# Optimization experiments

Measured on AMD Instinct MI355X. Metric: run time of the kernel, lower is better.

## Reference

```python
import jax, jax.numpy as jnp
import numpy as np

N = 100000
E = 1250000
D = 64
POS_DIM = 3


def _linear_params(key, fan_in, fan_out, bias=True):
    k1, k2 = jax.random.split(key)
    bound = 1.0 / np.sqrt(fan_in)
    W = jax.random.uniform(k1, (fan_in, fan_out), minval=-bound, maxval=bound, dtype=jnp.float32)
    if bias:
        b = jax.random.uniform(k2, (fan_out,), minval=-bound, maxval=bound, dtype=jnp.float32)
        return W, b
    return W


def setup_inputs() -> dict:
    key = jax.random.key(0)
    ks = jax.random.split(key, 10)
    x = jax.random.normal(ks[0], (N, D), dtype=jnp.float32)
    pos = jax.random.normal(ks[1], (N, POS_DIM), dtype=jnp.float32)
    edge_index = jax.random.randint(ks[2], (2, E), 0, N, dtype=jnp.int64)
    W_in, b_in = _linear_params(ks[3], D, D)
    W_lin = _linear_params(ks[4], D, D, bias=False)
    W_src = _linear_params(ks[5], D, D, bias=False)
    W_dst = _linear_params(ks[6], D, D, bias=False)
    W_pos, b_pos = _linear_params(ks[7], POS_DIM, D)
    W_out, b_out = _linear_params(ks[8], D, D)
    return {"x": x, "pos": pos, "edge_index": edge_index,
            "W_in": W_in, "b_in": b_in, "W_lin": W_lin, "W_src": W_src,
            "W_dst": W_dst, "W_pos": W_pos, "b_pos": b_pos,
            "W_out": W_out, "b_out": b_out}


def reference(x, pos, edge_index, W_in, b_in, W_lin, W_src, W_dst, W_pos, b_pos, W_out, b_out):
    n = x.shape[0]
    src, dst = edge_index[0], edge_index[1]  # j, i (PyG source_to_target)
    # lin_in + relu
    h = jax.nn.relu(x @ W_in + b_in)  # [N, D]
    # PointTransformerConv projections
    x_lin = h @ W_lin      # value projection, gathered at src (x_j)
    a_src = h @ W_src      # alpha_j side
    a_dst = h @ W_dst      # alpha_i side
    # per-edge positional MLP on pos_i - pos_j
    delta = (pos[dst] - pos[src]) @ W_pos + b_pos  # [E, D]
    # per-edge attention logits, per channel
    alpha = a_dst[dst] - a_src[src] + delta  # [E, D]
    # segment softmax over destination node groups (PyG softmax, eps=1e-16)
    seg_max = jax.ops.segment_max(alpha, dst, num_segments=n)
    alpha = jnp.exp(alpha - seg_max[dst])
    seg_sum = jax.ops.segment_sum(alpha, dst, num_segments=n)
    alpha = alpha / (seg_sum[dst] + 1e-16)
    # weighted messages, scatter-add aggregate
    msg = alpha * (x_lin[src] + delta)  # [E, D]
    out = jax.ops.segment_sum(msg, dst, num_segments=n)  # [N, D]
    # lin_out + relu
    return jax.nn.relu(out @ W_out + b_out)
```

## Files before the change

### kernel.cpp

```cpp
#include <hip/hip_runtime.h>

#define NN 100000
#define NE 1250000
#define NWIN 782
#define GA 256
#define CHUNK ((NE + GA - 1) / GA)
#define CAP 32
#define WEDCAP 40

typedef __attribute__((ext_vector_type(4))) float f32x4;
typedef __attribute__((ext_vector_type(8))) short s16x8;

__device__ __forceinline__ short bfb(float f) {
    union { float f; unsigned u; } c; c.f = f;
    unsigned u = c.u + 0x7fffu + ((c.u >> 16) & 1u);
    return (short)(u >> 16);
}
__device__ __forceinline__ void splitbf(float v, short& hi, short& lo) {
    hi = bfb(v);
    union { unsigned u; float f; } c; c.u = ((unsigned)(unsigned short)hi) << 16;
    lo = bfb(v - c.f);
}
__device__ __forceinline__ float lo2f(unsigned u) {
    union { unsigned u; float f; } c; c.u = u << 16; return c.f;
}
__device__ __forceinline__ float hi2f(unsigned u) {
    union { unsigned u; float f; } c; c.u = u & 0xffff0000u; return c.f;
}

__global__ __launch_bounds__(256) void k_prep(
    const float* __restrict__ Wi, const float* __restrict__ Wl,
    const float* __restrict__ Ws, const float* __restrict__ Wo,
    short* __restrict__ P)
{
    const int t = blockIdx.x * 256 + threadIdx.x;
    if (t >= 2048) return;
    const int mat = t >> 9, rem = t & 511;
    const int lane = rem & 63, cfg = rem >> 6;
    const int kh = cfg >> 2, nt = cfg & 3;
    const int m = lane & 15, q = lane >> 4;
    const float* W = mat == 0 ? Wi : mat == 1 ? Wl : mat == 2 ? Ws : Wo;
    s16x8 v;
    #pragma unroll
    for (int i = 0; i < 8; ++i)
        v[i] = bfb(W[(kh * 32 + q * 8 + i) * 64 + nt * 16 + m]);
    *(s16x8*)&P[(size_t)t * 8] = v;
}

__global__ __launch_bounds__(256) void k_node_in(
    const float* __restrict__ x, const short* __restrict__ P,
    const float* __restrict__ b_in, unsigned* __restrict__ AXb)
{
    __shared__ float hT[4][16 * 68];
    const int lane = threadIdx.x & 63;
    const int wid  = threadIdx.x >> 6;
    const int m = lane & 15, q = lane >> 4;

    s16x8 Wf[3][2][4];
    #pragma unroll
    for (int mat = 0; mat < 3; ++mat)
        #pragma unroll
        for (int kh = 0; kh < 2; ++kh)
            #pragma unroll
            for (int nt = 0; nt < 4; ++nt)
                Wf[mat][kh][nt] = *(const s16x8*)&P[((size_t)mat * 512 + (kh * 4 + nt) * 64 + lane) * 8];
    float bin[4];
    #pragma unroll
    for (int nt = 0; nt < 4; ++nt) bin[nt] = b_in[nt * 16 + m];

    const int wave = blockIdx.x * 4 + wid, nw = gridDim.x * 4;
    for (int chunk = wave; chunk < NN / 16; chunk += nw) {
        const int r0 = chunk * 16;
        const float* xr = x + (size_t)(r0 + m) * 64;
        float xv[16];
        *(float4*)&xv[0]  = *(const float4*)(xr + q * 8);
        *(float4*)&xv[4]  = *(const float4*)(xr + q * 8 + 4);
        *(float4*)&xv[8]  = *(const float4*)(xr + 32 + q * 8);
        *(float4*)&xv[12] = *(const float4*)(xr + 32 + q * 8 + 4);
        s16x8 ahi0, alo0, ahi1, alo1;
        #pragma unroll
        for (int i = 0; i < 8; ++i) {
            short h, l;
            splitbf(xv[i], h, l);     ahi0[i] = h; alo0[i] = l;
            splitbf(xv[8 + i], h, l); ahi1[i] = h; alo1[i] = l;
        }
        #pragma unroll
        for (int nt = 0; nt < 4; ++nt) {
            f32x4 acc = {0.f, 0.f, 0.f, 0.f};
            acc = __builtin_amdgcn_mfma_f32_16x16x32_bf16(alo0, Wf[0][0][nt], acc, 0, 0, 0);
            acc = __builtin_amdgcn_mfma_f32_16x16x32_bf16(alo1, Wf[0][1][nt], acc, 0, 0, 0);
            acc = __builtin_amdgcn_mfma_f32_16x16x32_bf16(ahi0, Wf[0][0][nt], acc, 0, 0, 0);
            acc = __builtin_amdgcn_mfma_f32_16x16x32_bf16(ahi1, Wf[0][1][nt], acc, 0, 0, 0);
            #pragma unroll
            for (int r = 0; r < 4; ++r) {
                float hv = acc[r] + bin[nt];
                hT[wid][(q * 4 + r) * 68 + nt * 16 + m] = hv > 0.f ? hv : 0.f;
            }
        }
        float hv[16];
        *(float4*)&hv[0]  = *(const float4*)&hT[wid][m * 68 + q * 8];
        *(float4*)&hv[4]  = *(const float4*)&hT[wid][m * 68 + q * 8 + 4];
        *(float4*)&hv[8]  = *(const float4*)&hT[wid][m * 68 + 32 + q * 8];
        *(float4*)&hv[12] = *(const float4*)&hT[wid][m * 68 + 32 + q * 8 + 4];
        s16x8 hhi0, hlo0, hhi1, hlo1;
        #pragma unroll
        for (int i = 0; i < 8; ++i) {
            short h, l;
            splitbf(hv[i], h, l);     hhi0[i] = h; hlo0[i] = l;
            splitbf(hv[8 + i], h, l); hhi1[i] = h; hlo1[i] = l;
        }
        #pragma unroll
        for (int nt = 0; nt < 4; ++nt) {
            f32x4 aS = {0.f, 0.f, 0.f, 0.f}, aL = {0.f, 0.f, 0.f, 0.f};
            aS = __builtin_amdgcn_mfma_f32_16x16x32_bf16(hlo0, Wf[2][0][nt], aS, 0, 0, 0);
            aS = __builtin_amdgcn_mfma_f32_16x16x32_bf16(hlo1, Wf[2][1][nt], aS, 0, 0, 0);
            aS = __builtin_amdgcn_mfma_f32_16x16x32_bf16(hhi0, Wf[2][0][nt], aS, 0, 0, 0);
            aS = __builtin_amdgcn_mfma_f32_16x16x32_bf16(hhi1, Wf[2][1][nt], aS, 0, 0, 0);
            aL = __builtin_amdgcn_mfma_f32_16x16x32_bf16(hlo0, Wf[1][0][nt], aL, 0, 0, 0);
            aL = __builtin_amdgcn_mfma_f32_16x16x32_bf16(hlo1, Wf[1][1][nt], aL, 0, 0, 0);
            aL = __builtin_amdgcn_mfma_f32_16x16x32_bf16(hhi0, Wf[1][0][nt], aL, 0, 0, 0);
            aL = __builtin_amdgcn_mfma_f32_16x16x32_bf16(hhi1, Wf[1][1][nt], aL, 0, 0, 0);
            #pragma unroll
            for (int r = 0; r < 4; ++r) {
                const unsigned p = (unsigned)(unsigned short)bfb(aS[r])
                                 | ((unsigned)(unsigned short)bfb(aL[r]) << 16);
                AXb[(size_t)(r0 + q * 4 + r) * 64 + nt * 16 + m] = p;
            }
        }
    }
}

__global__ __launch_bounds__(256) void k_passA(
    const int* __restrict__ ei, unsigned* __restrict__ stage, int* __restrict__ gcnt)
{
    __shared__ int lcnt[NWIN];
    const int g = blockIdx.x;
    for (int i = threadIdx.x; i < NWIN; i += 256) lcnt[i] = 0;
    __syncthreads();
    const int e0 = g * CHUNK;
    const int e1 = (e0 + CHUNK < NE) ? e0 + CHUNK : NE;
    for (int e = e0 + threadIdx.x; e < e1; e += 256) {
        const int s = ei[e], d = ei[NE + e];
        const int b = d >> 7;
        const int c = atomicAdd(&lcnt[b], 1);
        if (c < CAP)
            stage[((size_t)b * GA + g) * CAP + c] = (unsigned)s | ((unsigned)(d & 127) << 17);
    }
    __syncthreads();
    for (int i = threadIdx.x; i < NWIN; i += 256) gcnt[i * GA + g] = lcnt[i];
}

__global__ __launch_bounds__(256) void k_passB(
    const unsigned* __restrict__ stage, const int* __restrict__ gcnt,
    int* __restrict__ slots, int* __restrict__ deg)
{
    __shared__ int slotsL[128 * WEDCAP];
    __shared__ int cntL[128];
    const int b = blockIdx.x;
    const int t = threadIdx.x;
    if (t < 128) cntL[t] = 0;
    __syncthreads();
    int n = gcnt[b * GA + t]; n = n < CAP ? n : CAP;
    const unsigned* cell = stage + ((size_t)b * GA + t) * CAP;
    for (int i = 0; i < n; ++i) {
        const unsigned ent = cell[i];
        const int d7 = (int)(ent >> 17);
        const int c = atomicAdd(&cntL[d7], 1);
        if (c < WEDCAP) slotsL[d7 * WEDCAP + c] = (int)(ent & 0x1ffff);
    }
    __syncthreads();
    int4* dstq = (int4*)(slots + (size_t)b * 128 * WEDCAP);
    const int4* srcq = (const int4*)slotsL;
    #pragma unroll
    for (int i = 0; i < 5; ++i) dstq[i * 256 + t] = srcq[i * 256 + t];
    if (t < 128) {
        const int d = (b << 7) + t;
        if (d < NN) deg[d] = cntL[t] < WEDCAP ? cntL[t] : WEDCAP;
    }
}

__global__ __launch_bounds__(256) void k_agg(
    const int* __restrict__ deg_arr, const int* __restrict__ slots,
    const float* __restrict__ pos,
    const float* __restrict__ W_pos, const float* __restrict__ b_pos,
    const unsigned* __restrict__ AXb, float* __restrict__ V)
{
    const int lane = threadIdx.x & 63;
    const int d = __builtin_amdgcn_readfirstlane((int)((blockIdx.x * 256 + threadIdx.x) >> 6));
    if (d >= NN) return;
    const float wp0 = W_pos[lane], wp1 = W_pos[64 + lane], wp2 = W_pos[128 + lane];
    const float bp  = b_pos[lane];
    const float pd0 = pos[d * 3 + 0], pd1 = pos[d * 3 + 1], pd2 = pos[d * 3 + 2];

    int deg = deg_arr[d]; deg = deg < WEDCAP ? deg : WEDCAP;
    const int* srow = slots + (size_t)d * WEDCAP;

    float Sa = 0.f, Ua = 0.f;
    if (deg > 0) {
        int cs[4], ns[4];
        float cpx[4], cpy[4], cpz[4], npx[4], npy[4], npz[4];
        unsigned cax[4], nax[4];
        {
            const int4 qd = *(const int4*)srow;
            cs[0] = qd.x;
            cs[1] = (1 < deg) ? qd.y : qd.x;
            cs[2] = (2 < deg) ? qd.z : qd.x;
            cs[3] = (3 < deg) ? qd.w : qd.x;
            #pragma unroll
            for (int k = 0; k < 4; ++k) {
                cpx[k] = pos[cs[k] * 3 + 0];
                cpy[k] = pos[cs[k] * 3 + 1];
                cpz[k] = pos[cs[k] * 3 + 2];
                cax[k] = AXb[(size_t)cs[k] * 64 + lane];
            }
        }
        for (int j = 0; j < deg; j += 8) {
            if (j + 4 < deg) {
                const int4 qd = *(const int4*)(srow + j + 4);
                ns[0] = qd.x;
                ns[1] = (j + 5 < deg) ? qd.y : qd.x;
                ns[2] = (j + 6 < deg) ? qd.z : qd.x;
                ns[3] = (j + 7 < deg) ? qd.w : qd.x;
                #pragma unroll
                for (int k = 0; k < 4; ++k) {
                    npx[k] = pos[ns[k] * 3 + 0];
                    npy[k] = pos[ns[k] * 3 + 1];
                    npz[k] = pos[ns[k] * 3 + 2];
                    nax[k] = AXb[(size_t)ns[k] * 64 + lane];
                }
            }
            #pragma unroll
            for (int k = 0; k < 4; ++k) {
                const float dl = fmaf(pd0 - cpx[k], wp0,
                                 fmaf(pd1 - cpy[k], wp1,
                                 fmaf(pd2 - cpz[k], wp2, bp)));
                float wv = __expf(dl - lo2f(cax[k]));
                if (j + k >= deg) wv = 0.f;
                Sa += wv;
                Ua = fmaf(wv, hi2f(cax[k]) + dl, Ua);
            }
            if (j + 8 < deg) {
                const int4 qd = *(const int4*)(srow + j + 8);
                cs[0] = qd.x;
                cs[1] = (j + 9  < deg) ? qd.y : qd.x;
                cs[2] = (j + 10 < deg) ? qd.z : qd.x;
                cs[3] = (j + 11 < deg) ? qd.w : qd.x;
                #pragma unroll
                for (int k = 0; k < 4; ++k) {
                    cpx[k] = pos[cs[k] * 3 + 0];
                    cpy[k] = pos[cs[k] * 3 + 1];
                    cpz[k] = pos[cs[k] * 3 + 2];
                    cax[k] = AXb[(size_t)cs[k] * 64 + lane];
                }
            }
            if (j + 4 < deg) {
                #pragma unroll
                for (int k = 0; k < 4; ++k) {
                    const float dl = fmaf(pd0 - npx[k], wp0,
                                     fmaf(pd1 - npy[k], wp1,
                                     fmaf(pd2 - npz[k], wp2, bp)));
                    float wv = __expf(dl - lo2f(nax[k]));
                    if (j + 4 + k >= deg) wv = 0.f;
                    Sa += wv;
                    Ua = fmaf(wv, hi2f(nax[k]) + dl, Ua);
                }
            }
        }
    }
    V[(size_t)d * 64 + lane] = Ua / (Sa + 1e-16f);
}

__global__ __launch_bounds__(256) void k_node_out(
    const float* __restrict__ V, const short* __restrict__ P,
    const float* __restrict__ b_out, float* __restrict__ out)
{
    const int lane = threadIdx.x & 63;
    const int wid  = threadIdx.x >> 6;
    const int m = lane & 15, q = lane >> 4;

    s16x8 Wf[2][4];
    #pragma unroll
    for (int kh = 0; kh < 2; ++kh)
        #pragma unroll
        for (int nt = 0; nt < 4; ++nt)
            Wf[kh][nt] = *(const s16x8*)&P[((size_t)3 * 512 + (kh * 4 + nt) * 64 + lane) * 8];
    float bo[4];
    #pragma unroll
    for (int nt = 0; nt < 4; ++nt) bo[nt] = b_out[nt * 16 + m];

    const int wave = blockIdx.x * 4 + wid, nw = gridDim.x * 4;
    for (int chunk = wave; chunk < NN / 16; chunk += nw) {
        const int r0 = chunk * 16;
        const float* vr = V + (size_t)(r0 + m) * 64;
        float vv[16];
        *(float4*)&vv[0]  = *(const float4*)(vr + q * 8);
        *(float4*)&vv[4]  = *(const float4*)(vr + q * 8 + 4);
        *(float4*)&vv[8]  = *(const float4*)(vr + 32 + q * 8);
        *(float4*)&vv[12] = *(const float4*)(vr + 32 + q * 8 + 4);
        s16x8 ahi0, alo0, ahi1, alo1;
        #pragma unroll
        for (int i = 0; i < 8; ++i) {
            short h, l;
            splitbf(vv[i], h, l);     ahi0[i] = h; alo0[i] = l;
            splitbf(vv[8 + i], h, l); ahi1[i] = h; alo1[i] = l;
        }
        #pragma unroll
        for (int nt = 0; nt < 4; ++nt) {
            f32x4 acc = {0.f, 0.f, 0.f, 0.f};
            acc = __builtin_amdgcn_mfma_f32_16x16x32_bf16(alo0, Wf[0][nt], acc, 0, 0, 0);
            acc = __builtin_amdgcn_mfma_f32_16x16x32_bf16(alo1, Wf[1][nt], acc, 0, 0, 0);
            acc = __builtin_amdgcn_mfma_f32_16x16x32_bf16(ahi0, Wf[0][nt], acc, 0, 0, 0);
            acc = __builtin_amdgcn_mfma_f32_16x16x32_bf16(ahi1, Wf[1][nt], acc, 0, 0, 0);
            #pragma unroll
            for (int r = 0; r < 4; ++r) {
                float o = acc[r] + bo[nt];
                out[(size_t)(r0 + q * 4 + r) * 64 + nt * 16 + m] = o > 0.f ? o : 0.f;
            }
        }
    }
}

extern "C" void kernel_launch(void* const* d_in, const int* in_sizes, int n_in,
                              void* d_out, int out_size, void* d_ws, size_t ws_size,
                              hipStream_t stream) {
    const float* x     = (const float*)d_in[0];
    const float* pos   = (const float*)d_in[1];
    const int*   ei    = (const int*)d_in[2];
    const float* W_in  = (const float*)d_in[3];
    const float* b_in  = (const float*)d_in[4];
    const float* W_lin = (const float*)d_in[5];
    const float* W_src = (const float*)d_in[6];
    const float* W_pos = (const float*)d_in[8];
    const float* b_pos = (const float*)d_in[9];
    const float* W_out = (const float*)d_in[10];
    const float* b_out = (const float*)d_in[11];

    unsigned* AXb   = (unsigned*)d_ws;
    unsigned* stage = AXb + (size_t)NN * 64;
    int*      gcnt  = (int*)(stage + (size_t)NWIN * GA * CAP);
    int*      slots = gcnt + (size_t)NWIN * GA;
    int*      deg   = slots + (size_t)NWIN * 128 * WEDCAP;
    float*    V     = (float*)(deg + NN);
    short*    P     = (short*)(V + (size_t)NN * 64);

    k_prep    <<<8,    256, 0, stream>>>(W_in, W_lin, W_src, W_out, P);
    k_node_in <<<512,  256, 0, stream>>>(x, P, b_in, AXb);
    k_passA   <<<GA,   256, 0, stream>>>(ei, stage, gcnt);
    k_passB   <<<NWIN, 256, 0, stream>>>(stage, gcnt, slots, deg);
    k_agg     <<<(NN + 3) / 4, 256, 0, stream>>>(deg, slots, pos, W_pos, b_pos, AXb, V);
    k_node_out<<<512,  256, 0, stream>>>(V, P, b_out, (float*)d_out);
}
```

Before: 216.0 us.

## Fuse edge aggregation with output projection into one kernel per 16-node tile

Merges the per-node aggregation and the output linear+ReLU kernels. Each wave now aggregates 16 consecutive nodes sequentially, transposes them through shared memory, and applies the MFMA output projection directly. This removes the intermediate V buffer write/read and one launch. In exchange the grid shrinks 16x and each wave runs 16 serial latency-bound gather loops, reducing memory-level parallelism.

```diff
diff --git a/kernel.cpp b/kernel.cpp
--- a/kernel.cpp
+++ b/kernel.cpp
@@ -179,72 +179,54 @@
     }
 }
 
-__global__ __launch_bounds__(256) void k_agg(
+__global__ __launch_bounds__(256) void k_aggout(
     const int* __restrict__ deg_arr, const int* __restrict__ slots,
     const float* __restrict__ pos,
     const float* __restrict__ W_pos, const float* __restrict__ b_pos,
-    const unsigned* __restrict__ AXb, float* __restrict__ V)
-{
+    const unsigned* __restrict__ AXb,
+    const short* __restrict__ P, const float* __restrict__ b_out,
+    float* __restrict__ out)
+{
+    __shared__ float hT[4][16 * 68];
     const int lane = threadIdx.x & 63;
-    const int d = __builtin_amdgcn_readfirstlane((int)((blockIdx.x * 256 + threadIdx.x) >> 6));
-    if (d >= NN) return;
+    const int wid  = threadIdx.x >> 6;
+    const int m = lane & 15, q = lane >> 4;
+
+    const int gid = blockIdx.x * 4 + wid;
+    if (gid >= NN / 16) return;
+    const int dbase = gid * 16;
+
     const float wp0 = W_pos[lane], wp1 = W_pos[64 + lane], wp2 = W_pos[128 + lane];
     const float bp  = b_pos[lane];
-    const float pd0 = pos[d * 3 + 0], pd1 = pos[d * 3 + 1], pd2 = pos[d * 3 + 2];
-
-    int deg = deg_arr[d]; deg = deg < WEDCAP ? deg : WEDCAP;
-    const int* srow = slots + (size_t)d * WEDCAP;
-
-    float Sa = 0.f, Ua = 0.f;
-    if (deg > 0) {
-        int cs[4], ns[4];
-        float cpx[4], cpy[4], cpz[4], npx[4], npy[4], npz[4];
-        unsigned cax[4], nax[4];
-        {
-            const int4 qd = *(const int4*)srow;
-            cs[0] = qd.x;
-            cs[1] = (1 < deg) ? qd.y : qd.x;
-            cs[2] = (2 < deg) ? qd.z : qd.x;
-            cs[3] = (3 < deg) ? qd.w : qd.x;
-            #pragma unroll
-            for (int k = 0; k < 4; ++k) {
-                cpx[k] = pos[cs[k] * 3 + 0];
-                cpy[k] = pos[cs[k] * 3 + 1];
-                cpz[k] = pos[cs[k] * 3 + 2];
-                cax[k] = AXb[(size_t)cs[k] * 64 + lane];
-            }
-        }
-        for (int j = 0; j < deg; j += 8) {
-            if (j + 4 < deg) {
-                const int4 qd = *(const int4*)(srow + j + 4);
-                ns[0] = qd.x;
-                ns[1] = (j + 5 < deg) ? qd.y : qd.x;
-                ns[2] = (j + 6 < deg) ? qd.z : qd.x;
-                ns[3] = (j + 7 < deg) ? qd.w : qd.x;
-                #pragma unroll
-                for (int k = 0; k < 4; ++k) {
-                    npx[k] = pos[ns[k] * 3 + 0];
-                    npy[k] = pos[ns[k] * 3 + 1];
-                    npz[k] = pos[ns[k] * 3 + 2];
-                    nax[k] = AXb[(size_t)ns[k] * 64 + lane];
-                }
-            }
-            #pragma unroll
-            for (int k = 0; k < 4; ++k) {
-                const float dl = fmaf(pd0 - cpx[k], wp0,
-                                 fmaf(pd1 - cpy[k], wp1,
-                                 fmaf(pd2 - cpz[k], wp2, bp)));
-                float wv = __expf(dl - lo2f(cax[k]));
-                if (j + k >= deg) wv = 0.f;
-                Sa += wv;
-                Ua = fmaf(wv, hi2f(cax[k]) + dl, Ua);
-            }
-            if (j + 8 < deg) {
-                const int4 qd = *(const int4*)(srow + j + 8);
+    s16x8 Wf[2][4];
+    #pragma unroll
+    for (int kh = 0; kh < 2; ++kh)
+        #pragma unroll
+        for (int nt = 0; nt < 4; ++nt)
+            Wf[kh][nt] = *(const s16x8*)&P[((size_t)3 * 512 + (kh * 4 + nt) * 64 + lane) * 8];
+    float bo[4];
+    #pragma unroll
+    for (int nt = 0; nt < 4; ++nt) bo[nt] = b_out[nt * 16 + m];
+
+    float vreg[16];
+    #pragma unroll 1
+    for (int i = 0; i < 16; ++i) {
+        const int d = dbase + i;
+        int deg = deg_arr[d]; deg = deg < WEDCAP ? deg : WEDCAP;
+        const int* srow = slots + (size_t)d * WEDCAP;
+        const float pd0 = pos[d * 3 + 0], pd1 = pos[d * 3 + 1], pd2 = pos[d * 3 + 2];
+
+        float Sa = 0.f, Ua = 0.f;
+        if (deg > 0) {
+            int cs[4], ns[4];
+            float cpx[4], cpy[4], cpz[4], npx[4], npy[4], npz[4];
+            unsigned cax[4], nax[4];
+            {
+                const int4 qd = *(const int4*)srow;
                 cs[0] = qd.x;
-                cs[1] = (j + 9  < deg) ? qd.y : qd.x;
-                cs[2] = (j + 10 < deg) ? qd.z : qd.x;
-                cs[3] = (j + 11 < deg) ? qd.w : qd.x;
+                cs[1] = (1 < deg) ? qd.y : qd.x;
+                cs[2] = (2 < deg) ? qd.z : qd.x;
+                cs[3] = (3 < deg) ? qd.w : qd.x;
                 #pragma unroll
                 for (int k = 0; k < 4; ++k) {
                     cpx[k] = pos[cs[k] * 3 + 0];
@@ -253,69 +235,89 @@
                     cax[k] = AXb[(size_t)cs[k] * 64 + lane];
                 }
             }
-            if (j + 4 < deg) {
+            for (int j = 0; j < deg; j += 8) {
+                if (j + 4 < deg) {
+                    const int4 qd = *(const int4*)(srow + j + 4);
+                    ns[0] = qd.x;
+                    ns[1] = (j + 5 < deg) ? qd.y : qd.x;
+                    ns[2] = (j + 6 < deg) ? qd.z : qd.x;
+                    ns[3] = (j + 7 < deg) ? qd.w : qd.x;
+                    #pragma unroll
+                    for (int k = 0; k < 4; ++k) {
+                        npx[k] = pos[ns[k] * 3 + 0];
+                        npy[k] = pos[ns[k] * 3 + 1];
+                        npz[k] = pos[ns[k] * 3 + 2];
+                        nax[k] = AXb[(size_t)ns[k] * 64 + lane];
+                    }
+                }
                 #pragma unroll
                 for (int k = 0; k < 4; ++k) {
-                    const float dl = fmaf(pd0 - npx[k], wp0,
-                                     fmaf(pd1 - npy[k], wp1,
-                                     fmaf(pd2 - npz[k], wp2, bp)));
-                    float wv = __expf(dl - lo2f(nax[k]));
-                    if (j + 4 + k >= deg) wv = 0.f;
+                    const float dl = fmaf(pd0 - cpx[k], wp0,
+                                     fmaf(pd1 - cpy[k], wp1,
+                                     fmaf(pd2 - cpz[k], wp2, bp)));
+                    float wv = __expf(dl - lo2f(cax[k]));
+                    if (j + k >= deg) wv = 0.f;
                     Sa += wv;
-                    Ua = fmaf(wv, hi2f(nax[k]) + dl, Ua);
+                    Ua = fmaf(wv, hi2f(cax[k]) + dl, Ua);
+                }
+                if (j + 8 < deg) {
+                    const int4 qd = *(const int4*)(srow + j + 8);
+                    cs[0] = qd.x;
+                    cs[1] = (j + 9  < deg) ? qd.y : qd.x;
+                    cs[2] = (j + 10 < deg) ? qd.z : qd.x;
+                    cs[3] = (j + 11 < deg) ? qd.w : qd.x;
+                    #pragma unroll
+                    for (int k = 0; k < 4; ++k) {
+                        cpx[k] = pos[cs[k] * 3 + 0];
+                        cpy[k] = pos[cs[k] * 3 + 1];
+                        cpz[k] = pos[cs[k] * 3 + 2];
+                        cax[k] = AXb[(size_t)cs[k] * 64 + lane];
+                    }
+                }
+                if (j + 4 < deg) {
+                    #pragma unroll
+                    for (int k = 0; k < 4; ++k) {
+                        const float dl = fmaf(pd0 - npx[k], wp0,
+                                         fmaf(pd1 - npy[k], wp1,
+                                         fmaf(pd2 - npz[k], wp2, bp)));
+                        float wv = __expf(dl - lo2f(nax[k]));
+                        if (j + 4 + k >= deg) wv = 0.f;
+                        Sa += wv;
+                        Ua = fmaf(wv, hi2f(nax[k]) + dl, Ua);
+                    }
                 }
             }
         }
-    }
-    V[(size_t)d * 64 + lane] = Ua / (Sa + 1e-16f);
-}
-
-__global__ __launch_bounds__(256) void k_node_out(
-    const float* __restrict__ V, const short* __restrict__ P,
-    const float* __restrict__ b_out, float* __restrict__ out)
-{
-    const int lane = threadIdx.x & 63;
-    const int wid  = threadIdx.x >> 6;
-    const int m = lane & 15, q = lane >> 4;
-
-    s16x8 Wf[2][4];
-    #pragma unroll
-    for (int kh = 0; kh < 2; ++kh)
-        #pragma unroll
-        for (int nt = 0; nt < 4; ++nt)
-            Wf[kh][nt] = *(const s16x8*)&P[((size_t)3 * 512 + (kh * 4 + nt) * 64 + lane) * 8];
-    float bo[4];
-    #pragma unroll
-    for (int nt = 0; nt < 4; ++nt) bo[nt] = b_out[nt * 16 + m];
-
-    const int wave = blockIdx.x * 4 + wid, nw = gridDim.x * 4;
-    for (int chunk = wave; chunk < NN / 16; chunk += nw) {
-        const int r0 = chunk * 16;
-        const float* vr = V + (size_t)(r0 + m) * 64;
-        float vv[16];
-        *(float4*)&vv[0]  = *(const float4*)(vr + q * 8);
-        *(float4*)&vv[4]  = *(const float4*)(vr + q * 8 + 4);
-        *(float4*)&vv[8]  = *(const float4*)(vr + 32 + q * 8);
-        *(float4*)&vv[12] = *(const float4*)(vr + 32 + q * 8 + 4);
-        s16x8 ahi0, alo0, ahi1, alo1;
-        #pragma unroll
-        for (int i = 0; i < 8; ++i) {
-            short h, l;
-            splitbf(vv[i], h, l);     ahi0[i] = h; alo0[i] = l;
-            splitbf(vv[8 + i], h, l); ahi1[i] = h; alo1[i] = l;
-        }
-        #pragma unroll
-        for (int nt = 0; nt < 4; ++nt) {
-            f32x4 acc = {0.f, 0.f, 0.f, 0.f};
-            acc = __builtin_amdgcn_mfma_f32_16x16x32_bf16(alo0, Wf[0][nt], acc, 0, 0, 0);
-            acc = __builtin_amdgcn_mfma_f32_16x16x32_bf16(alo1, Wf[1][nt], acc, 0, 0, 0);
-            acc = __builtin_amdgcn_mfma_f32_16x16x32_bf16(ahi0, Wf[0][nt], acc, 0, 0, 0);
-            acc = __builtin_amdgcn_mfma_f32_16x16x32_bf16(ahi1, Wf[1][nt], acc, 0, 0, 0);
-            #pragma unroll
-            for (int r = 0; r < 4; ++r) {
-                float o = acc[r] + bo[nt];
-                out[(size_t)(r0 + q * 4 + r) * 64 + nt * 16 + m] = o > 0.f ? o : 0.f;
-            }
+        vreg[i] = Ua / (Sa + 1e-16f);
+    }
+
+    #pragma unroll
+    for (int i = 0; i < 16; ++i)
+        hT[wid][i * 68 + lane] = vreg[i];
+    float vv[16];
+    *(float4*)&vv[0]  = *(const float4*)&hT[wid][m * 68 + q * 8];
+    *(float4*)&vv[4]  = *(const float4*)&hT[wid][m * 68 + q * 8 + 4];
+    *(float4*)&vv[8]  = *(const float4*)&hT[wid][m * 68 + 32 + q * 8];
+    *(float4*)&vv[12] = *(const float4*)&hT[wid][m * 68 + 32 + q * 8 + 4];
+
+    s16x8 ahi0, alo0, ahi1, alo1;
+    #pragma unroll
+    for (int i = 0; i < 8; ++i) {
+        short h, l;
+        splitbf(vv[i], h, l);     ahi0[i] = h; alo0[i] = l;
+        splitbf(vv[8 + i], h, l); ahi1[i] = h; alo1[i] = l;
+    }
+    #pragma unroll
+    for (int nt = 0; nt < 4; ++nt) {
+        f32x4 acc = {0.f, 0.f, 0.f, 0.f};
+        acc = __builtin_amdgcn_mfma_f32_16x16x32_bf16(alo0, Wf[0][nt], acc, 0, 0, 0);
+        acc = __builtin_amdgcn_mfma_f32_16x16x32_bf16(alo1, Wf[1][nt], acc, 0, 0, 0);
+        acc = __builtin_amdgcn_mfma_f32_16x16x32_bf16(ahi0, Wf[0][nt], acc, 0, 0, 0);
+        acc = __builtin_amdgcn_mfma_f32_16x16x32_bf16(ahi1, Wf[1][nt], acc, 0, 0, 0);
+        #pragma unroll
+        for (int r = 0; r < 4; ++r) {
+            const float o = acc[r] + bo[nt];
+            out[(size_t)(dbase + q * 4 + r) * 64 + nt * 16 + m] = o > 0.f ? o : 0.f;
         }
     }
 }
@@ -340,13 +342,11 @@
     int*      gcnt  = (int*)(stage + (size_t)NWIN * GA * CAP);
     int*      slots = gcnt + (size_t)NWIN * GA;
     int*      deg   = slots + (size_t)NWIN * 128 * WEDCAP;
-    float*    V     = (float*)(deg + NN);
-    short*    P     = (short*)(V + (size_t)NN * 64);
-
-    k_prep    <<<8,    256, 0, stream>>>(W_in, W_lin, W_src, W_out, P);
-    k_node_in <<<512,  256, 0, stream>>>(x, P, b_in, AXb);
-    k_passA   <<<GA,   256, 0, stream>>>(ei, stage, gcnt);
-    k_passB   <<<NWIN, 256, 0, stream>>>(stage, gcnt, slots, deg);
-    k_agg     <<<(NN + 3) / 4, 256, 0, stream>>>(deg, slots, pos, W_pos, b_pos, AXb, V);
-    k_node_out<<<512,  256, 0, stream>>>(V, P, b_out, (float*)d_out);
-}
+    short*    P     = (short*)(deg + NN);
+
+    k_prep   <<<8,    256, 0, stream>>>(W_in, W_lin, W_src, W_out, P);
+    k_node_in<<<512,  256, 0, stream>>>(x, P, b_in, AXb);
+    k_passA  <<<GA,   256, 0, stream>>>(ei, stage, gcnt);
+    k_passB  <<<NWIN, 256, 0, stream>>>(stage, gcnt, slots, deg);
+    k_aggout <<<(NN / 16 + 3) / 4, 256, 0, stream>>>(deg, slots, pos, W_pos, b_pos, AXb, P, b_out, (float*)d_out);
+}
```

New measurement: 289.1 us. +33.9%, slower.

## Shrink edge staging cells to 16 with global overflow list and per-block layout

Applied to the files above, without the earlier changes.

The per-window edge staging buffer is cut from 32 to 16 slots per cell, and each passA block now writes to its own contiguous region instead of interleaving cells by window. Edges that overflow a cell go to a global overflow list through an atomic counter, and every passB block scans that list for its window's entries. passB reads each cell with four vector loads and an unrolled loop. This shrinks the staging footprint and gives passA writes better locality, at the cost of a global atomic on overflow and a full overflow scan in every passB block.

```diff
diff --git a/kernel.cpp b/kernel.cpp
--- a/kernel.cpp
+++ b/kernel.cpp
@@ -5,7 +5,8 @@
 #define NWIN 782
 #define GA 256
 #define CHUNK ((NE + GA - 1) / GA)
-#define CAP 32
+#define CAP16 16
+#define OVFCAP 131072
 #define WEDCAP 40
 
 typedef __attribute__((ext_vector_type(4))) float f32x4;
@@ -31,9 +32,10 @@
 __global__ __launch_bounds__(256) void k_prep(
     const float* __restrict__ Wi, const float* __restrict__ Wl,
     const float* __restrict__ Ws, const float* __restrict__ Wo,
-    short* __restrict__ P)
+    short* __restrict__ P, int* __restrict__ ovf_cnt)
 {
     const int t = blockIdx.x * 256 + threadIdx.x;
+    if (t == 0) *ovf_cnt = 0;
     if (t >= 2048) return;
     const int mat = t >> 9, rem = t & 511;
     const int lane = rem & 63, cfg = rem >> 6;
@@ -131,27 +133,35 @@
 }
 
 __global__ __launch_bounds__(256) void k_passA(
-    const int* __restrict__ ei, unsigned* __restrict__ stage, int* __restrict__ gcnt)
+    const int* __restrict__ ei, unsigned* __restrict__ stage, int* __restrict__ gcnt,
+    int2* __restrict__ ovf, int* __restrict__ ovf_cnt)
 {
     __shared__ int lcnt[NWIN];
     const int g = blockIdx.x;
     for (int i = threadIdx.x; i < NWIN; i += 256) lcnt[i] = 0;
     __syncthreads();
+    unsigned* myStage = stage + (size_t)g * NWIN * CAP16;
     const int e0 = g * CHUNK;
     const int e1 = (e0 + CHUNK < NE) ? e0 + CHUNK : NE;
     for (int e = e0 + threadIdx.x; e < e1; e += 256) {
         const int s = ei[e], d = ei[NE + e];
         const int b = d >> 7;
         const int c = atomicAdd(&lcnt[b], 1);
-        if (c < CAP)
-            stage[((size_t)b * GA + g) * CAP + c] = (unsigned)s | ((unsigned)(d & 127) << 17);
+        if (c < CAP16) {
+            myStage[b * CAP16 + c] = (unsigned)s | ((unsigned)(d & 127) << 17);
+        } else {
+            const int o = atomicAdd(ovf_cnt, 1);
+            if (o < OVFCAP) ovf[o] = make_int2(s, d);
+        }
     }
     __syncthreads();
-    for (int i = threadIdx.x; i < NWIN; i += 256) gcnt[i * GA + g] = lcnt[i];
+    for (int i = threadIdx.x; i < NWIN; i += 256)
+        gcnt[i * GA + g] = lcnt[i] < CAP16 ? lcnt[i] : CAP16;
 }
 
 __global__ __launch_bounds__(256) void k_passB(
     const unsigned* __restrict__ stage, const int* __restrict__ gcnt,
+    const int2* __restrict__ ovf, const int* __restrict__ ovf_cnt,
     int* __restrict__ slots, int* __restrict__ deg)
 {
     __shared__ int slotsL[128 * WEDCAP];
@@ -160,13 +170,29 @@
     const int t = threadIdx.x;
     if (t < 128) cntL[t] = 0;
     __syncthreads();
-    int n = gcnt[b * GA + t]; n = n < CAP ? n : CAP;
-    const unsigned* cell = stage + ((size_t)b * GA + t) * CAP;
-    for (int i = 0; i < n; ++i) {
-        const unsigned ent = cell[i];
-        const int d7 = (int)(ent >> 17);
-        const int c = atomicAdd(&cntL[d7], 1);
-        if (c < WEDCAP) slotsL[d7 * WEDCAP + c] = (int)(ent & 0x1ffff);
+    const int n = min(gcnt[b * GA + t], CAP16);
+    const unsigned* cell = stage + (size_t)t * NWIN * CAP16 + b * CAP16;
+    uint4 q0 = *(const uint4*)cell;
+    uint4 q1 = *(const uint4*)(cell + 4);
+    uint4 q2 = *(const uint4*)(cell + 8);
+    uint4 q3 = *(const uint4*)(cell + 12);
+    const unsigned eb[16] = {q0.x, q0.y, q0.z, q0.w, q1.x, q1.y, q1.z, q1.w,
+                             q2.x, q2.y, q2.z, q2.w, q3.x, q3.y, q3.z, q3.w};
+    #pragma unroll
+    for (int i = 0; i < CAP16; ++i)
+        if (i < n) {
+            const int d7 = (int)(eb[i] >> 17);
+            const int c = atomicAdd(&cntL[d7], 1);
+            if (c < WEDCAP) slotsL[d7 * WEDCAP + c] = (int)(eb[i] & 0x1ffff);
+        }
+    const int no = min(*ovf_cnt, OVFCAP);
+    for (int i = t; i < no; i += 256) {
+        const int2 sd = ovf[i];
+        if ((sd.y >> 7) == b) {
+            const int d7 = sd.y & 127;
+            const int c = atomicAdd(&cntL[d7], 1);
+            if (c < WEDCAP) slotsL[d7 * WEDCAP + c] = sd.x;
+        }
     }
     __syncthreads();
     int4* dstq = (int4*)(slots + (size_t)b * 128 * WEDCAP);
@@ -337,16 +363,18 @@
 
     unsigned* AXb   = (unsigned*)d_ws;
     unsigned* stage = AXb + (size_t)NN * 64;
-    int*      gcnt  = (int*)(stage + (size_t)NWIN * GA * CAP);
+    int*      gcnt  = (int*)(stage + (size_t)GA * NWIN * CAP16);
     int*      slots = gcnt + (size_t)NWIN * GA;
     int*      deg   = slots + (size_t)NWIN * 128 * WEDCAP;
     float*    V     = (float*)(deg + NN);
-    short*    P     = (short*)(V + (size_t)NN * 64);
-
-    k_prep    <<<8,    256, 0, stream>>>(W_in, W_lin, W_src, W_out, P);
+    int2*     ovf   = (int2*)(V + (size_t)NN * 64);
+    int*      ovfc  = (int*)(ovf + OVFCAP);
+    short*    P     = (short*)(ovfc + 64);
+
+    k_prep    <<<8,    256, 0, stream>>>(W_in, W_lin, W_src, W_out, P, ovfc);
     k_node_in <<<512,  256, 0, stream>>>(x, P, b_in, AXb);
-    k_passA   <<<GA,   256, 0, stream>>>(ei, stage, gcnt);
-    k_passB   <<<NWIN, 256, 0, stream>>>(stage, gcnt, slots, deg);
+    k_passA   <<<GA,   256, 0, stream>>>(ei, stage, gcnt, ovf, ovfc);
+    k_passB   <<<NWIN, 256, 0, stream>>>(stage, gcnt, ovf, ovfc, slots, deg);
     k_agg     <<<(NN + 3) / 4, 256, 0, stream>>>(deg, slots, pos, W_pos, b_pos, AXb, V);
     k_node_out<<<512,  256, 0, stream>>>(V, P, b_out, (float*)d_out);
 }
```

After: 205.9 us. -4.7%, faster.
